# Kernel tuning notes

Hardware: AMD Instinct MI355X
Metric: run time of the kernel (lower is better)

The kernel has to match this reference:

```python
import jax, jax.numpy as jnp
import numpy as np

EMBED_DIM = 1024
NUM_HEADS = 16
HEAD_DIM = EMBED_DIM // NUM_HEADS


def setup_inputs() -> dict:
    key = jax.random.key(0)
    k_x, k_wqkv, k_bqkv, k_wp, k_bp = jax.random.split(key, 5)
    B, S = 4, 2048
    scale = 1.0 / np.sqrt(EMBED_DIM)
    return {
        "x": jax.random.normal(k_x, (B, S, EMBED_DIM), dtype=jnp.float32),
        "w_qkv": jax.random.uniform(k_wqkv, (EMBED_DIM, 3 * EMBED_DIM), jnp.float32, -scale, scale),
        "b_qkv": jax.random.uniform(k_bqkv, (3 * EMBED_DIM,), jnp.float32, -scale, scale),
        "w_proj": jax.random.uniform(k_wp, (EMBED_DIM, EMBED_DIM), jnp.float32, -scale, scale),
        "b_proj": jax.random.uniform(k_bp, (EMBED_DIM,), jnp.float32, -scale, scale),
    }


def reference(x, w_qkv, b_qkv, w_proj, b_proj):
    B, S, E = x.shape
    H, D = NUM_HEADS, HEAD_DIM
    # fused QKV projection: [B,S,3E] -> [3,B,H,S,D]
    qkv = (x @ w_qkv + b_qkv).reshape(B, S, 3, H, D).transpose(2, 0, 3, 1, 4)
    q, k, v = qkv[0], qkv[1], qkv[2]
    scores = jnp.einsum("bhqd,bhkd->bhqk", q, k) / np.sqrt(D).astype(jnp.float32)
    attn = jax.nn.softmax(scores, axis=-1)  # dropout is identity in eval
    out = jnp.einsum("bhqk,bhkd->bhqd", attn, v)
    out = out.transpose(0, 2, 1, 3).reshape(B, S, E)
    return out @ w_proj + b_proj
```

## Files before the change

### kernel.cpp

```cpp
#include <hip/hip_runtime.h>
#include <hip/hip_bf16.h>

#define PB 4
#define PS 2048
#define PH 16
#define PD 64
#define PE 1024

typedef short v8s __attribute__((ext_vector_type(8)));
typedef float v4f __attribute__((ext_vector_type(4)));

__device__ __forceinline__ ushort f2b(float f) {
  union { __hip_bfloat16 b; ushort u; } cv;
  cv.b = __float2bfloat16(f);
  return cv.u;
}

__device__ __forceinline__ void cp16(const __hip_bfloat16* g, __hip_bfloat16* l) {
  __builtin_amdgcn_global_load_lds(
      (const __attribute__((address_space(1))) void*)g,
      (__attribute__((address_space(3))) void*)l, 16, 0, 0);
}

__global__ __launch_bounds__(256) void conv_f2b(const float* __restrict__ S,
                                                __hip_bfloat16* __restrict__ D) {
  int i = blockIdx.x * 256 + threadIdx.x;
  float4 f = reinterpret_cast<const float4*>(S)[i];
  union { ushort u[4]; uint2 v; } pk;
  pk.u[0] = f2b(f.x); pk.u[1] = f2b(f.y); pk.u[2] = f2b(f.z); pk.u[3] = f2b(f.w);
  reinterpret_cast<uint2*>(D)[i] = pk.v;
}

__global__ __launch_bounds__(256) void transp_f2b(const float* __restrict__ S,
                                                  __hip_bfloat16* __restrict__ D,
                                                  int R, int C) {
  __shared__ float tile[32][33];
  const int t = threadIdx.x;
  const int tx = t & 31, ty = t >> 5;
  const int r0 = blockIdx.y * 32, c0 = blockIdx.x * 32;
#pragma unroll
  for (int i = 0; i < 4; ++i)
    tile[ty + 8 * i][tx] = S[(size_t)(r0 + ty + 8 * i) * C + c0 + tx];
  __syncthreads();
#pragma unroll
  for (int i = 0; i < 4; ++i)
    D[(size_t)(c0 + ty + 8 * i) * R + r0 + tx] = __float2bfloat16(tile[tx][ty + 8 * i]);
}

template <int MODE>
__global__ __launch_bounds__(256) void gemm_bt(
    const __hip_bfloat16* __restrict__ A, const __hip_bfloat16* __restrict__ BT,
    const float* __restrict__ bias, void* __restrict__ outv) {
  __shared__ __hip_bfloat16 As[128 * 64];
  __shared__ __hip_bfloat16 Bs[128 * 64];
  const int t = threadIdx.x;
  const int lane = t & 63, w = t >> 6;
  const int ln = lane & 15, qd = lane >> 4;
  const int wm = w >> 1, wn = w & 1;
  const int m0 = blockIdx.y * 128, n0 = blockIdx.x * 128;
  v4f acc[4][4] = {};

  for (int k0 = 0; k0 < PE; k0 += 64) {
    __syncthreads();
#pragma unroll
    for (int i = 0; i < 4; ++i) {
      int idx = t + 256 * i;
      int r = idx >> 3, cs = idx & 7;
      int cg = cs ^ (r & 7);
      cp16(A + (size_t)(m0 + r) * PE + k0 + cg * 8, As + idx * 8);
      cp16(BT + (size_t)(n0 + r) * PE + k0 + cg * 8, Bs + idx * 8);
    }
    __syncthreads();
#pragma unroll
    for (int kk = 0; kk < 2; ++kk) {
      v8s af[4], bf[4];
#pragma unroll
      for (int mb = 0; mb < 4; ++mb) {
        int ra = wm * 64 + mb * 16 + ln;
        int ca = (kk * 4 + qd) ^ (ra & 7);
        af[mb] = *reinterpret_cast<const v8s*>(As + ra * 64 + ca * 8);
      }
#pragma unroll
      for (int nb = 0; nb < 4; ++nb) {
        int rb = wn * 64 + nb * 16 + ln;
        int cb = (kk * 4 + qd) ^ (rb & 7);
        bf[nb] = *reinterpret_cast<const v8s*>(Bs + rb * 64 + cb * 8);
      }
#pragma unroll
      for (int mb = 0; mb < 4; ++mb)
#pragma unroll
        for (int nb = 0; nb < 4; ++nb)
          acc[mb][nb] = __builtin_amdgcn_mfma_f32_16x16x32_bf16(af[mb], bf[nb],
                                                                acc[mb][nb], 0, 0, 0);
    }
  }

  const int mwb = m0 + wm * 64 + qd * 4;
  const int nwb = n0 + wn * 64 + ln;
  if (MODE == 0) {
    __hip_bfloat16* QKV = (__hip_bfloat16*)outv;
#pragma unroll
    for (int nb = 0; nb < 4; ++nb) {
      int n = nwb + nb * 16;
      float bv = bias[n];
      int which = n >> 10, h = (n >> 6) & 15, d = n & 63;
#pragma unroll
      for (int mb = 0; mb < 4; ++mb) {
        int r0 = mwb + mb * 16;
        int b = r0 >> 11, s0 = r0 & (PS - 1);
        v4f a = acc[mb][nb];
        if (which == 2) {
          union { ushort u[4]; uint2 v; } pk;
#pragma unroll
          for (int i = 0; i < 4; ++i) pk.u[i] = f2b(a[i] + bv);
          size_t idx = (((size_t)(2 * PB + b) * PH + h) * PD + d) * PS + s0;
          *reinterpret_cast<uint2*>(&QKV[idx]) = pk.v;
        } else {
          float sc = (which == 0) ? 0.125f : 1.0f;
          size_t base = (((size_t)(which * PB + b) * PH + h) * PS + s0) * PD + d;
#pragma unroll
          for (int i = 0; i < 4; ++i)
            QKV[base + (size_t)i * PD] = __float2bfloat16((a[i] + bv) * sc);
        }
      }
    }
  } else {
    float* Co = (float*)outv;
#pragma unroll
    for (int nb = 0; nb < 4; ++nb) {
      int n = nwb + nb * 16;
      float bv = bias[n];
#pragma unroll
      for (int mb = 0; mb < 4; ++mb) {
        int r0 = mwb + mb * 16;
        v4f a = acc[mb][nb];
#pragma unroll
        for (int i = 0; i < 4; ++i)
          Co[(size_t)(r0 + i) * PE + n] = a[i] + bv;
      }
    }
  }
}

__global__ __launch_bounds__(256) void attn_mfma3(
    const __hip_bfloat16* __restrict__ QKV, __hip_bfloat16* __restrict__ O) {
  __shared__ __hip_bfloat16 Ks[128 * 64];
  __shared__ __hip_bfloat16 Vts[64 * 128];
  __shared__ __hip_bfloat16 Ps[128][136];
  const int t = threadIdx.x;
  const int lane = t & 63, w = t >> 6;
  const int ln = lane & 15, qd = lane >> 4;
  const int b = blockIdx.y >> 4, h = blockIdx.y & 15;
  const int q0 = blockIdx.x * 128;
  const __hip_bfloat16* Qb = QKV + (size_t)(b * PH + h) * PS * PD;
  const __hip_bfloat16* Kb = QKV + (size_t)((PB + b) * PH + h) * PS * PD;
  const __hip_bfloat16* Vb = QKV + (size_t)((2 * PB + b) * PH + h) * PD * PS;

  v8s qf[2][2];
#pragma unroll
  for (int u = 0; u < 2; ++u) {
    size_t qr = (size_t)(q0 + 32 * w + 16 * u + ln) * PD;
    qf[u][0] = *reinterpret_cast<const v8s*>(Qb + qr + qd * 8);
    qf[u][1] = *reinterpret_cast<const v8s*>(Qb + qr + 32 + qd * 8);
  }
  v4f oacc[2][4] = {};
  float lrow[2] = {0.f, 0.f};

  for (int kt = 0; kt < PS; kt += 128) {
    __syncthreads();
#pragma unroll
    for (int i = 0; i < 4; ++i) {
      int idx = t + 256 * i;
      int rk = idx >> 3, ck = (idx & 7) ^ (rk & 7);
      cp16(Kb + (size_t)(kt + rk) * PD + ck * 8, Ks + idx * 8);
      int rv = idx >> 4, cv = (idx & 15) ^ (rv & 7);
      cp16(Vb + (size_t)rv * PS + kt + cv * 8, Vts + idx * 8);
    }
    __syncthreads();

#pragma unroll
    for (int u = 0; u < 2; ++u) {
      float psum = 0.f;
#pragma unroll
      for (int nb = 0; nb < 8; ++nb) {
        int nr = nb * 16 + ln;
        int c0 = qd ^ (nr & 7);
        v8s k0 = *reinterpret_cast<const v8s*>(Ks + nr * 64 + c0 * 8);
        v8s k1 = *reinterpret_cast<const v8s*>(Ks + nr * 64 + (c0 ^ 4) * 8);
        v4f z = {};
        z = __builtin_amdgcn_mfma_f32_16x16x32_bf16(k0, qf[u][0], z, 0, 0, 0);
        v4f sv = __builtin_amdgcn_mfma_f32_16x16x32_bf16(k1, qf[u][1], z, 0, 0, 0);
        union { ushort pu[4]; uint2 pv; } pk;
#pragma unroll
        for (int i = 0; i < 4; ++i) {
          float p = __expf(sv[i]);
          psum += p;
          pk.pu[i] = f2b(p);
        }
        *reinterpret_cast<uint2*>(&Ps[32 * w + 16 * u + ln][nb * 16 + qd * 4]) = pk.pv;
      }
      psum += __shfl_xor(psum, 16);
      psum += __shfl_xor(psum, 32);
      lrow[u] += psum;
    }
    v8s pf[2][4];
#pragma unroll
    for (int u = 0; u < 2; ++u)
#pragma unroll
      for (int s = 0; s < 4; ++s)
        pf[u][s] = *reinterpret_cast<const v8s*>(
            &Ps[32 * w + 16 * u + ln][s * 32 + qd * 8]);
#pragma unroll
    for (int db = 0; db < 4; ++db) {
      int rv = db * 16 + ln;
      v4f o0 = oacc[0][db], o1 = oacc[1][db];
#pragma unroll
      for (int s = 0; s < 4; ++s) {
        int cv = (s * 4 + qd) ^ (rv & 7);
        v8s vf = *reinterpret_cast<const v8s*>(Vts + rv * 128 + cv * 8);
        o0 = __builtin_amdgcn_mfma_f32_16x16x32_bf16(pf[0][s], vf, o0, 0, 0, 0);
        o1 = __builtin_amdgcn_mfma_f32_16x16x32_bf16(pf[1][s], vf, o1, 0, 0, 0);
      }
      oacc[0][db] = o0;
      oacc[1][db] = o1;
    }
  }
#pragma unroll
  for (int u = 0; u < 2; ++u) {
#pragma unroll
    for (int i = 0; i < 4; ++i) {
      float inv = 1.f / __shfl(lrow[u], qd * 4 + i);
      int sg = q0 + 32 * w + 16 * u + qd * 4 + i;
      size_t base = (((size_t)b * PS + sg) * PH + h) * PD;
#pragma unroll
      for (int db = 0; db < 4; ++db)
        O[base + db * 16 + ln] = __float2bfloat16(oacc[u][db][i] * inv);
    }
  }
}

__device__ __forceinline__ uint2 load4bf(const float* p) {
  const float4 f = *reinterpret_cast<const float4*>(p);
  union { ushort u[4]; uint2 v; } pk;
  pk.u[0] = f2b(f.x); pk.u[1] = f2b(f.y); pk.u[2] = f2b(f.z); pk.u[3] = f2b(f.w);
  return pk.v;
}
__device__ __forceinline__ uint2 load4bf(const __hip_bfloat16* p) {
  return *reinterpret_cast<const uint2*>(p);
}

template <typename AT, int MODE>
__global__ __launch_bounds__(256) void gemm128(
    const AT* __restrict__ A, const float* __restrict__ Bm,
    const float* __restrict__ bias, void* __restrict__ outv, int ldb) {
  __shared__ __hip_bfloat16 As[128][40];
  __shared__ __hip_bfloat16 Bs[128][40];
  const int t = threadIdx.x;
  const int lane = t & 63, w = t >> 6;
  const int ln = lane & 15, qd = lane >> 4;
  const int wm = w >> 1, wn = w & 1;
  const int m0 = blockIdx.y * 128, n0 = blockIdx.x * 128;
  v4f acc[4][4] = {};
  for (int k0 = 0; k0 < PE; k0 += 32) {
    __syncthreads();
#pragma unroll
    for (int i = 0; i < 4; ++i) {
      int p = t + 256 * i;
      int m = p >> 3, kc = p & 7;
      *reinterpret_cast<uint2*>(&As[m][kc * 4]) =
          load4bf(A + (size_t)(m0 + m) * PE + k0 + kc * 4);
    }
#pragma unroll
    for (int i = 0; i < 4; ++i) {
      int p = t + 256 * i;
      int n = p & 127, kc = p >> 7;
      union { ushort u[4]; uint2 v; } pk;
#pragma unroll
      for (int r = 0; r < 4; ++r)
        pk.u[r] = f2b(Bm[(size_t)(k0 + kc * 4 + r) * ldb + n0 + n]);
      *reinterpret_cast<uint2*>(&Bs[n][kc * 4]) = pk.v;
    }
    __syncthreads();
    v8s af[4], bf[4];
#pragma unroll
    for (int mb = 0; mb < 4; ++mb)
      af[mb] = *reinterpret_cast<const v8s*>(&As[wm * 64 + mb * 16 + ln][qd * 8]);
#pragma unroll
    for (int nb = 0; nb < 4; ++nb)
      bf[nb] = *reinterpret_cast<const v8s*>(&Bs[wn * 64 + nb * 16 + ln][qd * 8]);
#pragma unroll
    for (int mb = 0; mb < 4; ++mb)
#pragma unroll
      for (int nb = 0; nb < 4; ++nb)
        acc[mb][nb] = __builtin_amdgcn_mfma_f32_16x16x32_bf16(af[mb], bf[nb],
                                                              acc[mb][nb], 0, 0, 0);
  }
  const int mwb = m0 + wm * 64 + qd * 4;
  const int nwb = n0 + wn * 64 + ln;
  if (MODE == 0) {
    __hip_bfloat16* QKV = (__hip_bfloat16*)outv;
#pragma unroll
    for (int nb = 0; nb < 4; ++nb) {
      int n = nwb + nb * 16;
      float bv = bias[n];
      int which = n >> 10, h = (n >> 6) & 15, d = n & 63;
#pragma unroll
      for (int mb = 0; mb < 4; ++mb) {
        int r0 = mwb + mb * 16;
        int b = r0 >> 11, s0 = r0 & (PS - 1);
        v4f a = acc[mb][nb];
        if (which == 2) {
          union { ushort u[4]; uint2 v; } pk;
#pragma unroll
          for (int i = 0; i < 4; ++i) pk.u[i] = f2b(a[i] + bv);
          size_t idx = (((size_t)(2 * PB + b) * PH + h) * PD + d) * PS + s0;
          *reinterpret_cast<uint2*>(&QKV[idx]) = pk.v;
        } else {
          float sc = (which == 0) ? 0.125f : 1.0f;
          size_t base = (((size_t)(which * PB + b) * PH + h) * PS + s0) * PD + d;
#pragma unroll
          for (int i = 0; i < 4; ++i)
            QKV[base + (size_t)i * PD] = __float2bfloat16((a[i] + bv) * sc);
        }
      }
    }
  } else {
    float* Co = (float*)outv;
#pragma unroll
    for (int nb = 0; nb < 4; ++nb) {
      int n = nwb + nb * 16;
      float bv = bias[n];
#pragma unroll
      for (int mb = 0; mb < 4; ++mb) {
        int r0 = mwb + mb * 16;
        v4f a = acc[mb][nb];
#pragma unroll
        for (int i = 0; i < 4; ++i)
          Co[(size_t)(r0 + i) * PE + n] = a[i] + bv;
      }
    }
  }
}

extern "C" void kernel_launch(void* const* d_in, const int* in_sizes, int n_in,
                              void* d_out, int out_size, void* d_ws,
                              size_t ws_size, hipStream_t stream) {
  const float* x = (const float*)d_in[0];
  const float* w_qkv = (const float*)d_in[1];
  const float* b_qkv = (const float*)d_in[2];
  const float* w_proj = (const float*)d_in[3];
  const float* b_proj = (const float*)d_in[4];
  float* out = (float*)d_out;

  const size_t xE = (size_t)PB * PS * PE;
  const size_t wqE = (size_t)PE * 3 * PE;
  const size_t wpE = (size_t)PE * PE;
  const size_t qkvE = (size_t)3 * PB * PH * PS * PD;
  const size_t needMain = (xE + wqE + wpE + qkvE) * 2;

  dim3 blk(256);
  dim3 gq(24, 64), ga(16, 64), gp(8, 64);

  if (ws_size >= needMain) {
    __hip_bfloat16* xb = (__hip_bfloat16*)d_ws;
    __hip_bfloat16* wqkvT = xb + xE;
    __hip_bfloat16* wprojT = wqkvT + wqE;
    __hip_bfloat16* qkv = wprojT + wpE;
    __hip_bfloat16* o = xb;

    conv_f2b<<<dim3(xE / 1024), blk, 0, stream>>>(x, xb);
    transp_f2b<<<dim3(96, 32), blk, 0, stream>>>(w_qkv, wqkvT, PE, 3 * PE);
    transp_f2b<<<dim3(32, 32), blk, 0, stream>>>(w_proj, wprojT, PE, PE);
    gemm_bt<0><<<gq, blk, 0, stream>>>(xb, wqkvT, b_qkv, qkv);
    attn_mfma3<<<ga, blk, 0, stream>>>(qkv, o);
    gemm_bt<1><<<gp, blk, 0, stream>>>(o, wprojT, b_proj, out);
  } else {
    __hip_bfloat16* qkv = (__hip_bfloat16*)d_ws;
    if (ws_size >= (qkvE + xE) * 2) {
      __hip_bfloat16* o = qkv + qkvE;
      gemm128<float, 0><<<gq, blk, 0, stream>>>(x, w_qkv, b_qkv, qkv, 3 * PE);
      attn_mfma3<<<ga, blk, 0, stream>>>(qkv, o);
      gemm128<__hip_bfloat16, 1><<<gp, blk, 0, stream>>>(o, w_proj, b_proj, out, PE);
    } else {
      __hip_bfloat16* o = (__hip_bfloat16*)d_out;
      float* tmp = (float*)d_ws;
      gemm128<float, 0><<<gq, blk, 0, stream>>>(x, w_qkv, b_qkv, qkv, 3 * PE);
      attn_mfma3<<<ga, blk, 0, stream>>>(qkv, o);
      gemm128<__hip_bfloat16, 1><<<gp, blk, 0, stream>>>(o, w_proj, b_proj, tmp, PE);
      hipMemcpyAsync(d_out, tmp, xE * sizeof(float), hipMemcpyDeviceToDevice, stream);
    }
  }
}
```

Baseline: 308.2 us.

## Keep softmax probabilities in registers and fold log2e into Q scale

The attention kernel no longer writes the exponentiated scores to a shared-memory P tile and reads them back as MFMA operands. It packs them straight into register fragments and permutes the V reads so the k index matches the register layout of the score MFMA output. The Q scale now also includes log2(e), so the kernel can call a hardware exp2 instead of exp. This removes the LDS round trip and the larger shared allocation, which may help occupancy, at the cost of more register pressure and 8-byte V loads from LDS.

Measured after the change: 286.9 us. 6.9% less time.

```diff
diff --git a/kernel.cpp b/kernel.cpp
--- a/kernel.cpp
+++ b/kernel.cpp
@@ -10,11 +10,19 @@
 typedef short v8s __attribute__((ext_vector_type(8)));
 typedef float v4f __attribute__((ext_vector_type(4)));
 
+#define QSCALE 0.18033688f
+
 __device__ __forceinline__ ushort f2b(float f) {
   union { __hip_bfloat16 b; ushort u; } cv;
   cv.b = __float2bfloat16(f);
   return cv.u;
 }
+
+#if __has_builtin(__builtin_amdgcn_exp2f)
+__device__ __forceinline__ float fexp2(float x) { return __builtin_amdgcn_exp2f(x); }
+#else
+__device__ __forceinline__ float fexp2(float x) { return exp2f(x); }
+#endif
 
 __device__ __forceinline__ void cp16(const __hip_bfloat16* g, __hip_bfloat16* l) {
   __builtin_amdgcn_global_load_lds(
@@ -116,7 +124,7 @@
           size_t idx = (((size_t)(2 * PB + b) * PH + h) * PD + d) * PS + s0;
           *reinterpret_cast<uint2*>(&QKV[idx]) = pk.v;
         } else {
-          float sc = (which == 0) ? 0.125f : 1.0f;
+          float sc = (which == 0) ? QSCALE : 1.0f;
           size_t base = (((size_t)(which * PB + b) * PH + h) * PS + s0) * PD + d;
 #pragma unroll
           for (int i = 0; i < 4; ++i)
@@ -142,11 +150,10 @@
   }
 }
 
-__global__ __launch_bounds__(256) void attn_mfma3(
+__global__ __launch_bounds__(256) void attn_mfma4(
     const __hip_bfloat16* __restrict__ QKV, __hip_bfloat16* __restrict__ O) {
   __shared__ __hip_bfloat16 Ks[128 * 64];
   __shared__ __hip_bfloat16 Vts[64 * 128];
-  __shared__ __hip_bfloat16 Ps[128][136];
   const int t = threadIdx.x;
   const int lane = t & 63, w = t >> 6;
   const int ln = lane & 15, qd = lane >> 4;
@@ -178,6 +185,7 @@
     }
     __syncthreads();
 
+    uint2 pw[2][8];
 #pragma unroll
     for (int u = 0; u < 2; ++u) {
       float psum = 0.f;
@@ -193,36 +201,35 @@
         union { ushort pu[4]; uint2 pv; } pk;
 #pragma unroll
         for (int i = 0; i < 4; ++i) {
-          float p = __expf(sv[i]);
+          float p = fexp2(sv[i]);
           psum += p;
           pk.pu[i] = f2b(p);
         }
-        *reinterpret_cast<uint2*>(&Ps[32 * w + 16 * u + ln][nb * 16 + qd * 4]) = pk.pv;
+        pw[u][nb] = pk.pv;
       }
       psum += __shfl_xor(psum, 16);
       psum += __shfl_xor(psum, 32);
       lrow[u] += psum;
     }
-    v8s pf[2][4];
-#pragma unroll
-    for (int u = 0; u < 2; ++u)
-#pragma unroll
-      for (int s = 0; s < 4; ++s)
-        pf[u][s] = *reinterpret_cast<const v8s*>(
-            &Ps[32 * w + 16 * u + ln][s * 32 + qd * 8]);
-#pragma unroll
-    for (int db = 0; db < 4; ++db) {
-      int rv = db * 16 + ln;
-      v4f o0 = oacc[0][db], o1 = oacc[1][db];
-#pragma unroll
-      for (int s = 0; s < 4; ++s) {
-        int cv = (s * 4 + qd) ^ (rv & 7);
-        v8s vf = *reinterpret_cast<const v8s*>(Vts + rv * 128 + cv * 8);
-        o0 = __builtin_amdgcn_mfma_f32_16x16x32_bf16(pf[0][s], vf, o0, 0, 0, 0);
-        o1 = __builtin_amdgcn_mfma_f32_16x16x32_bf16(pf[1][s], vf, o1, 0, 0, 0);
-      }
-      oacc[0][db] = o0;
-      oacc[1][db] = o1;
+
+#pragma unroll
+    for (int s = 0; s < 4; ++s) {
+      union { v8s v; uint2 u2[2]; } a0, a1;
+      a0.u2[0] = pw[0][2 * s]; a0.u2[1] = pw[0][2 * s + 1];
+      a1.u2[0] = pw[1][2 * s]; a1.u2[1] = pw[1][2 * s + 1];
+#pragma unroll
+      for (int db = 0; db < 4; ++db) {
+        int rv = db * 16 + ln;
+        const uint2* vrow = reinterpret_cast<const uint2*>(Vts + rv * 128);
+        int L0 = 4 * s + (qd >> 1);
+        union { v8s v; uint2 u2[2]; } vf;
+        vf.u2[0] = vrow[((L0 ^ (rv & 7)) << 1) | (qd & 1)];
+        vf.u2[1] = vrow[(((L0 + 2) ^ (rv & 7)) << 1) | (qd & 1)];
+        oacc[0][db] = __builtin_amdgcn_mfma_f32_16x16x32_bf16(a0.v, vf.v,
+                                                              oacc[0][db], 0, 0, 0);
+        oacc[1][db] = __builtin_amdgcn_mfma_f32_16x16x32_bf16(a1.v, vf.v,
+                                                              oacc[1][db], 0, 0, 0);
+      }
     }
   }
 #pragma unroll
@@ -316,7 +323,7 @@
           size_t idx = (((size_t)(2 * PB + b) * PH + h) * PD + d) * PS + s0;
           *reinterpret_cast<uint2*>(&QKV[idx]) = pk.v;
         } else {
-          float sc = (which == 0) ? 0.125f : 1.0f;
+          float sc = (which == 0) ? QSCALE : 1.0f;
           size_t base = (((size_t)(which * PB + b) * PH + h) * PS + s0) * PD + d;
 #pragma unroll
           for (int i = 0; i < 4; ++i)
@@ -372,20 +379,20 @@
     transp_f2b<<<dim3(96, 32), blk, 0, stream>>>(w_qkv, wqkvT, PE, 3 * PE);
     transp_f2b<<<dim3(32, 32), blk, 0, stream>>>(w_proj, wprojT, PE, PE);
     gemm_bt<0><<<gq, blk, 0, stream>>>(xb, wqkvT, b_qkv, qkv);
-    attn_mfma3<<<ga, blk, 0, stream>>>(qkv, o);
+    attn_mfma4<<<ga, blk, 0, stream>>>(qkv, o);
     gemm_bt<1><<<gp, blk, 0, stream>>>(o, wprojT, b_proj, out);
   } else {
     __hip_bfloat16* qkv = (__hip_bfloat16*)d_ws;
     if (ws_size >= (qkvE + xE) * 2) {
       __hip_bfloat16* o = qkv + qkvE;
       gemm128<float, 0><<<gq, blk, 0, stream>>>(x, w_qkv, b_qkv, qkv, 3 * PE);
-      attn_mfma3<<<ga, blk, 0, stream>>>(qkv, o);
+      attn_mfma4<<<ga, blk, 0, stream>>>(qkv, o);
       gemm128<__hip_bfloat16, 1><<<gp, blk, 0, stream>>>(o, w_proj, b_proj, out, PE);
     } else {
       __hip_bfloat16* o = (__hip_bfloat16*)d_out;
       float* tmp = (float*)d_ws;
       gemm128<float, 0><<<gq, blk, 0, stream>>>(x, w_qkv, b_qkv, qkv, 3 * PE);
-      attn_mfma3<<<ga, blk, 0, stream>>>(qkv, o);
+      attn_mfma4<<<ga, blk, 0, stream>>>(qkv, o);
       gemm128<__hip_bfloat16, 1><<<gp, blk, 0, stream>>>(o, w_proj, b_proj, tmp, PE);
       hipMemcpyAsync(d_out, tmp, xE * sizeof(float), hipMemcpyDeviceToDevice, stream);
     }
```
